# Kernel tuning notes

Hardware: AMD Instinct MI355X
Metric: run time of the kernel (lower is better)

## Reference

```python
import jax, jax.numpy as jnp
import numpy as np

K_TOP = 2  # top-k experts per token (MoE k)


def setup_inputs() -> dict:
    key = jax.random.key(0)
    ks = jax.random.split(key, 4)
    B, D, H, E = 4096, 1024, 2048, 8
    x = jax.random.normal(ks[0], (B, D), dtype=jnp.float32)
    w_gate = jax.random.normal(ks[1], (D, E), dtype=jnp.float32) * 0.02
    W1 = jax.random.normal(ks[2], (E, D, H), dtype=jnp.float32) * (1.0 / np.sqrt(D))
    b1 = jnp.zeros((E, H), dtype=jnp.float32)
    W2 = jax.random.normal(ks[3], (E, H, D), dtype=jnp.float32) * (1.0 / np.sqrt(H))
    b2 = jnp.zeros((E, D), dtype=jnp.float32)
    return {"x": x, "w_gate": w_gate, "W1": W1, "b1": b1, "W2": W2, "b2": b2}


def _top_k_gates(logits, k):
    # noisy_top_k_gating, eval path (noisy_gating=False / train=False):
    # softmax over the top-k logits, scattered back to [B, E]; other gates are 0.
    B, E = logits.shape
    top_logits, top_idx = jax.lax.top_k(logits, k)       # [B, k]
    top_gates = jax.nn.softmax(top_logits, axis=-1)      # [B, k]
    rows = jnp.arange(B)[:, None]
    gates = jnp.zeros((B, E), dtype=logits.dtype).at[rows, top_idx].set(top_gates)
    return gates


def reference(x, w_gate, W1, b1, W2, b2):
    # Gating
    logits = x @ w_gate                                  # [B, E]
    gates = _top_k_gates(logits, K_TOP)                  # [B, E], sparse (top-k nonzero)
    # Experts: MLP(fc1 -> relu -> fc2) per expert. Dense-all-experts form is
    # mathematically identical to dispatch/combine since zero gates contribute 0.
    h = jax.nn.relu(jnp.einsum('bd,edh->beh', x, W1) + b1[None])   # [B, E, H]
    y = jnp.einsum('beh,ehd->bed', h, W2) + b2[None]               # [B, E, D]
    out = jnp.einsum('be,bed->bd', gates, y)                       # gated scatter-combine
    return out
```

## Files before the change

### kernel.cpp

```cpp
#include <hip/hip_runtime.h>

#define B_TOK 4096
#define DDIM  1024
#define HDIM  2048
#define NEXP  8
#define MAXTOK 4096
#define BK 64
#define BM1 64
#define BN1 128
#define BM2 64
#define BN2 128

#define OFF_W1T  0ull
#define OFF_W2T  33554432ull
#define OFF_XB   67108864ull
#define OFF_H    75497472ull
#define OFF_Y    109051904ull
#define OFF_TOK  125829120ull
#define OFF_GATE 125960192ull
#define OFF_PAIR 126091264ull
#define OFF_CNT  126124032ull
#define OFF_OFFS 126124096ull
#define OFF_EIDX (OFF_Y)
#define OFF_GCO  (OFF_Y + 16384ull)

typedef __attribute__((ext_vector_type(4))) float f32x4;
typedef __attribute__((ext_vector_type(8))) short bf16x8;

static __device__ __forceinline__ unsigned short f2bf(float f) {
    unsigned u = __builtin_bit_cast(unsigned, f);
    unsigned r = (u + 0x7FFFu + ((u >> 16) & 1u)) >> 16;
    return (unsigned short)r;
}
static __device__ __forceinline__ float bf2f(unsigned short s) {
    unsigned u = ((unsigned)s) << 16;
    return __builtin_bit_cast(float, u);
}

#define AS1(p) ((const __attribute__((address_space(1))) void*)(p))
#define AS3(p) ((__attribute__((address_space(3))) void*)(p))

__global__ void __launch_bounds__(256) gating_logits_kernel(
    const float* __restrict__ x, const float* __restrict__ wg,
    int* __restrict__ eidx, float* __restrict__ gco, short* __restrict__ Xb) {
    int wave = threadIdx.x >> 6;
    int lane = threadIdx.x & 63;
    int b = blockIdx.x * 4 + wave;
    float acc[NEXP];
#pragma unroll
    for (int e = 0; e < NEXP; e++) acc[e] = 0.f;
    const float* xr = x + (size_t)b * DDIM;
    short* xbr = Xb + (size_t)b * DDIM;
#pragma unroll
    for (int i = 0; i < DDIM / 64; i++) {
        int d = i * 64 + lane;
        float xv = xr[d];
        xbr[d] = (short)f2bf(xv);
        const float4* wrow = (const float4*)(wg + (size_t)d * NEXP);
        float4 w0 = wrow[0], w1 = wrow[1];
        acc[0] += xv * w0.x; acc[1] += xv * w0.y; acc[2] += xv * w0.z; acc[3] += xv * w0.w;
        acc[4] += xv * w1.x; acc[5] += xv * w1.y; acc[6] += xv * w1.z; acc[7] += xv * w1.w;
    }
#pragma unroll
    for (int off = 32; off >= 1; off >>= 1)
#pragma unroll
        for (int e = 0; e < NEXP; e++) acc[e] += __shfl_xor(acc[e], off);
    if (lane == 0) {
        int i1 = 0; float m1 = acc[0];
        for (int e = 1; e < NEXP; e++) if (acc[e] > m1) { m1 = acc[e]; i1 = e; }
        int i2 = (i1 == 0) ? 1 : 0; float m2 = -1e30f;
        for (int e = 0; e < NEXP; e++) { if (e == i1) continue; if (acc[e] > m2) { m2 = acc[e]; i2 = e; } }
        float g1 = 1.f / (1.f + expf(m2 - m1));
        eidx[b] = i1 | (i2 << 16);
        gco[b] = g1;
    }
}

__global__ void __launch_bounds__(256) build_kernel(
    const int* __restrict__ eidx, const float* __restrict__ gco,
    int* __restrict__ counts, int* __restrict__ tok,
    float* __restrict__ gate, int* __restrict__ pair) {
    __shared__ int lhist[NEXP];
    __shared__ int gbase[NEXP];
    int t = threadIdx.x;
    if (t < NEXP) lhist[t] = 0;
    __syncthreads();
    int b = blockIdx.x * 256 + t;
    int ep = eidx[b];
    int e1 = ep & 0xffff, e2 = ep >> 16;
    float g1 = gco[b], g2 = 1.f - g1;
    int l1 = atomicAdd(&lhist[e1], 1);
    int l2 = atomicAdd(&lhist[e2], 1);
    __syncthreads();
    if (t < NEXP) gbase[t] = atomicAdd(&counts[t], lhist[t]);
    __syncthreads();
    int s1 = gbase[e1] + l1, s2 = gbase[e2] + l2;
    tok[e1 * MAXTOK + s1] = b; gate[e1 * MAXTOK + s1] = g1; pair[b * 2 + 0] = e1 * MAXTOK + s1;
    tok[e2 * MAXTOK + s2] = b; gate[e2 * MAXTOK + s2] = g2; pair[b * 2 + 1] = e2 * MAXTOK + s2;
}

__global__ void scan_kernel(const int* __restrict__ counts, int* __restrict__ offs) {
    if (threadIdx.x == 0) {
        int s = 0;
        for (int e = 0; e < NEXP; e++) { offs[e] = s; s += counts[e]; }
    }
}

__global__ void __launch_bounds__(256) tcvt_kernel(const float* __restrict__ src, short* __restrict__ dst,
                                                   int R, int C) {
    __shared__ float tile[64][65];
    int e = blockIdx.z;
    size_t base = (size_t)e * R * C;
    int r0 = blockIdx.y * 64, c0 = blockIdx.x * 64;
    int t = threadIdx.x;
    int rr = t >> 4, c4 = (t & 15) * 4;
    const float* s = src + base + (size_t)r0 * C + c0;
#pragma unroll
    for (int i = 0; i < 4; i++) {
        float4 v = *(const float4*)(s + (size_t)(rr + i * 16) * C + c4);
        tile[rr + i * 16][c4 + 0] = v.x; tile[rr + i * 16][c4 + 1] = v.y;
        tile[rr + i * 16][c4 + 2] = v.z; tile[rr + i * 16][c4 + 3] = v.w;
    }
    __syncthreads();
    short* d = dst + base + (size_t)c0 * R + r0;
    int hr0 = t >> 4, dc = (t & 15) * 4;
#pragma unroll
    for (int i = 0; i < 4; i++) {
        int hr = hr0 + i * 16;
        short4 o;
        o.x = (short)f2bf(tile[dc + 0][hr]); o.y = (short)f2bf(tile[dc + 1][hr]);
        o.z = (short)f2bf(tile[dc + 2][hr]); o.w = (short)f2bf(tile[dc + 3][hr]);
        *(short4*)(d + (size_t)hr * R + dc) = o;
    }
}

__global__ void __launch_bounds__(256, 4) fc1_kernel(
    const short* __restrict__ Xb, const short* __restrict__ W1T, const float* __restrict__ b1,
    short* __restrict__ h, const int* __restrict__ tok,
    const int* __restrict__ counts, const int* __restrict__ offs) {
    int bid = blockIdx.x;
    int e = bid & 7;
    int r2 = bid >> 3;
    int m0 = (r2 & 63) * BM1;
    int n0 = (r2 >> 6) * BN1;
    int cnt = counts[e];
    if (m0 >= cnt) return;
    int baseh = offs[e];

    __shared__ short As[BM1 * BK];
    __shared__ short Bs[BN1 * BK];

    int t = threadIdx.x;
    int wave = t >> 6, lane = t & 63;

    const short* asrc[2]; int dstoA[2];
    const short* bsrc[4]; int dstoB[4];
#pragma unroll
    for (int i = 0; i < 2; i++) {
        int G = i * 256 + t;
        int r = G >> 3, q = G & 7;
        int cks = ((q ^ (r & 7)) << 3);
        int trow = m0 + r;
        int tid2 = (trow < cnt) ? tok[e * MAXTOK + trow] : 0;
        asrc[i] = Xb + (size_t)tid2 * DDIM + cks;
        dstoA[i] = G * 8;
    }
#pragma unroll
    for (int i = 0; i < 4; i++) {
        int G = i * 256 + t;
        int r = G >> 3, q = G & 7;
        int cks = ((q ^ (r & 7)) << 3);
        bsrc[i] = W1T + ((size_t)e * HDIM + n0 + r) * DDIM + cks;
        dstoB[i] = G * 8;
    }

    int wr = (wave >> 1) * 32, wc = (wave & 1) * 64;
    f32x4 acc[2][4];
    f32x4 zero = {0.f, 0.f, 0.f, 0.f};
#pragma unroll
    for (int m = 0; m < 2; m++)
#pragma unroll
        for (int n = 0; n < 4; n++) acc[m][n] = zero;

    int l15 = lane & 15, l7 = lane & 7, lhi = lane >> 4;
    int aoff[2][2], boff[4][2];
#pragma unroll
    for (int ks = 0; ks < 2; ks++) {
        int q = (lhi + ks * 4) ^ l7;
#pragma unroll
        for (int m = 0; m < 2; m++) aoff[m][ks] = (wr + m * 16 + l15) * BK + (q << 3);
#pragma unroll
        for (int n = 0; n < 4; n++) boff[n][ks] = (wc + n * 16 + l15) * BK + (q << 3);
    }

    const int NT = DDIM / BK;
    for (int kt = 0; kt < NT; ++kt) {
        int k0 = kt * BK;
#pragma unroll
        for (int i = 0; i < 2; i++)
            __builtin_amdgcn_global_load_lds(AS1(asrc[i] + k0), AS3(&As[dstoA[i]]), 16, 0, 0);
#pragma unroll
        for (int i = 0; i < 4; i++)
            __builtin_amdgcn_global_load_lds(AS1(bsrc[i] + k0), AS3(&Bs[dstoB[i]]), 16, 0, 0);
        __syncthreads();
#pragma unroll
        for (int ks = 0; ks < 2; ks++) {
            bf16x8 af[2], bg[4];
#pragma unroll
            for (int m = 0; m < 2; m++) af[m] = *(const bf16x8*)(&As[aoff[m][ks]]);
#pragma unroll
            for (int n = 0; n < 4; n++) bg[n] = *(const bf16x8*)(&Bs[boff[n][ks]]);
            __builtin_amdgcn_s_setprio(1);
#pragma unroll
            for (int m = 0; m < 2; m++)
#pragma unroll
                for (int n = 0; n < 4; n++)
                    acc[m][n] = __builtin_amdgcn_mfma_f32_16x16x32_bf16(bg[n], af[m], acc[m][n], 0, 0, 0);
            __builtin_amdgcn_s_setprio(0);
        }
        __syncthreads();
    }

#pragma unroll
    for (int m = 0; m < 2; m++) {
        int row = m0 + wr + m * 16 + l15;
        if (row < cnt) {
            size_t rb = (size_t)(baseh + row) * HDIM;
#pragma unroll
            for (int n = 0; n < 4; n++) {
                int colb = n0 + wc + n * 16 + (lhi << 2);
                float4 bias = *(const float4*)(b1 + e * HDIM + colb);
                float v0 = acc[m][n][0] + bias.x; v0 = v0 > 0.f ? v0 : 0.f;
                float v1 = acc[m][n][1] + bias.y; v1 = v1 > 0.f ? v1 : 0.f;
                float v2 = acc[m][n][2] + bias.z; v2 = v2 > 0.f ? v2 : 0.f;
                float v3 = acc[m][n][3] + bias.w; v3 = v3 > 0.f ? v3 : 0.f;
                short4 o;
                o.x = (short)f2bf(v0); o.y = (short)f2bf(v1);
                o.z = (short)f2bf(v2); o.w = (short)f2bf(v3);
                *(short4*)(h + rb + colb) = o;
            }
        }
    }
}

__global__ void __launch_bounds__(256, 4) fc2_kernel(
    const short* __restrict__ h, const short* __restrict__ W2T, const float* __restrict__ b2,
    short* __restrict__ ybuf, const int* __restrict__ counts, const int* __restrict__ offs) {
    int bid = blockIdx.x;
    int e = bid & 7;
    int r2 = bid >> 3;
    int m0 = (r2 & 63) * BM2;
    int n0 = (r2 >> 6) * BN2;
    int cnt = counts[e];
    if (m0 >= cnt) return;
    int baseh = offs[e];

    __shared__ short As[BM2 * BK];
    __shared__ short Bs[BN2 * BK];

    int t = threadIdx.x;
    int wave = t >> 6, lane = t & 63;

    const short* asrc[2]; int dstoA[2];
    const short* bsrc[4]; int dstoB[4];
#pragma unroll
    for (int i = 0; i < 2; i++) {
        int G = i * 256 + t;
        int r = G >> 3, q = G & 7;
        int cks = ((q ^ (r & 7)) << 3);
        asrc[i] = h + (size_t)(baseh + m0 + r) * HDIM + cks;
        dstoA[i] = G * 8;
    }
#pragma unroll
    for (int i = 0; i < 4; i++) {
        int G = i * 256 + t;
        int r = G >> 3, q = G & 7;
        int cks = ((q ^ (r & 7)) << 3);
        bsrc[i] = W2T + ((size_t)e * DDIM + n0 + r) * HDIM + cks;
        dstoB[i] = G * 8;
    }

    int wr = (wave >> 1) * 32, wc = (wave & 1) * 64;
    f32x4 acc[2][4];
    f32x4 zero = {0.f, 0.f, 0.f, 0.f};
#pragma unroll
    for (int m = 0; m < 2; m++)
#pragma unroll
        for (int n = 0; n < 4; n++) acc[m][n] = zero;

    int l15 = lane & 15, l7 = lane & 7, lhi = lane >> 4;
    int aoff[2][2], boff[4][2];
#pragma unroll
    for (int ks = 0; ks < 2; ks++) {
        int q = (lhi + ks * 4) ^ l7;
#pragma unroll
        for (int m = 0; m < 2; m++) aoff[m][ks] = (wr + m * 16 + l15) * BK + (q << 3);
#pragma unroll
        for (int n = 0; n < 4; n++) boff[n][ks] = (wc + n * 16 + l15) * BK + (q << 3);
    }

    const int NT = HDIM / BK;
    for (int kt = 0; kt < NT; ++kt) {
        int k0 = kt * BK;
#pragma unroll
        for (int i = 0; i < 2; i++)
            __builtin_amdgcn_global_load_lds(AS1(asrc[i] + k0), AS3(&As[dstoA[i]]), 16, 0, 0);
#pragma unroll
        for (int i = 0; i < 4; i++)
            __builtin_amdgcn_global_load_lds(AS1(bsrc[i] + k0), AS3(&Bs[dstoB[i]]), 16, 0, 0);
        __syncthreads();
#pragma unroll
        for (int ks = 0; ks < 2; ks++) {
            bf16x8 af[2], bg[4];
#pragma unroll
            for (int m = 0; m < 2; m++) af[m] = *(const bf16x8*)(&As[aoff[m][ks]]);
#pragma unroll
            for (int n = 0; n < 4; n++) bg[n] = *(const bf16x8*)(&Bs[boff[n][ks]]);
            __builtin_amdgcn_s_setprio(1);
#pragma unroll
            for (int m = 0; m < 2; m++)
#pragma unroll
                for (int n = 0; n < 4; n++)
                    acc[m][n] = __builtin_amdgcn_mfma_f32_16x16x32_bf16(bg[n], af[m], acc[m][n], 0, 0, 0);
            __builtin_amdgcn_s_setprio(0);
        }
        __syncthreads();
    }

#pragma unroll
    for (int m = 0; m < 2; m++) {
        int row = m0 + wr + m * 16 + l15;
        if (row < cnt) {
            size_t rb = (size_t)(baseh + row) * DDIM;
#pragma unroll
            for (int n = 0; n < 4; n++) {
                int colb = n0 + wc + n * 16 + (lhi << 2);
                float4 bias = *(const float4*)(b2 + e * DDIM + colb);
                short4 o;
                o.x = (short)f2bf(acc[m][n][0] + bias.x);
                o.y = (short)f2bf(acc[m][n][1] + bias.y);
                o.z = (short)f2bf(acc[m][n][2] + bias.z);
                o.w = (short)f2bf(acc[m][n][3] + bias.w);
                *(short4*)(ybuf + rb + colb) = o;
            }
        }
    }
}

__global__ void __launch_bounds__(256) combine_kernel(
    const short* __restrict__ ybuf, const float* __restrict__ gate,
    const int* __restrict__ pair, const int* __restrict__ offs, float* __restrict__ out) {
    int b = blockIdx.x;
    int p0 = pair[b * 2], p1 = pair[b * 2 + 1];
    float g0 = gate[p0], g1 = gate[p1];
    int r0 = offs[p0 >> 12] + (p0 & 4095);
    int r1 = offs[p1 >> 12] + (p1 & 4095);
    const short4* y0 = (const short4*)(ybuf + (size_t)r0 * DDIM);
    const short4* y1 = (const short4*)(ybuf + (size_t)r1 * DDIM);
    float4* o = (float4*)(out + (size_t)b * DDIM);
    int t = threadIdx.x;
    short4 a = y0[t], c = y1[t];
    float4 v;
    v.x = g0 * bf2f((unsigned short)a.x) + g1 * bf2f((unsigned short)c.x);
    v.y = g0 * bf2f((unsigned short)a.y) + g1 * bf2f((unsigned short)c.y);
    v.z = g0 * bf2f((unsigned short)a.z) + g1 * bf2f((unsigned short)c.z);
    v.w = g0 * bf2f((unsigned short)a.w) + g1 * bf2f((unsigned short)c.w);
    o[t] = v;
}

extern "C" void kernel_launch(void* const* d_in, const int* in_sizes, int n_in,
                              void* d_out, int out_size, void* d_ws, size_t ws_size,
                              hipStream_t stream) {
    const float* x  = (const float*)d_in[0];
    const float* wg = (const float*)d_in[1];
    const float* W1 = (const float*)d_in[2];
    const float* b1 = (const float*)d_in[3];
    const float* W2 = (const float*)d_in[4];
    const float* b2 = (const float*)d_in[5];
    float* out = (float*)d_out;
    char* ws = (char*)d_ws;

    short* W1T = (short*)(ws + OFF_W1T);
    short* W2T = (short*)(ws + OFF_W2T);
    short* Xb  = (short*)(ws + OFF_XB);
    short* h   = (short*)(ws + OFF_H);
    short* ybuf = (short*)(ws + OFF_Y);
    int* tok   = (int*)(ws + OFF_TOK);
    float* gate = (float*)(ws + OFF_GATE);
    int* pair  = (int*)(ws + OFF_PAIR);
    int* counts = (int*)(ws + OFF_CNT);
    int* offs  = (int*)(ws + OFF_OFFS);
    int* eidx  = (int*)(ws + OFF_EIDX);
    float* gco = (float*)(ws + OFF_GCO);

    hipMemsetAsync(counts, 0, 64, stream);
    gating_logits_kernel<<<B_TOK / 4, 256, 0, stream>>>(x, wg, eidx, gco, Xb);
    build_kernel<<<B_TOK / 256, 256, 0, stream>>>(eidx, gco, counts, tok, gate, pair);
    scan_kernel<<<1, 64, 0, stream>>>(counts, offs);
    tcvt_kernel<<<dim3(HDIM / 64, DDIM / 64, NEXP), 256, 0, stream>>>(W1, W1T, DDIM, HDIM);
    tcvt_kernel<<<dim3(DDIM / 64, HDIM / 64, NEXP), 256, 0, stream>>>(W2, W2T, HDIM, DDIM);
    fc1_kernel<<<NEXP * (MAXTOK / BM1) * (HDIM / BN1), 256, 0, stream>>>(Xb, W1T, b1, h, tok, counts, offs);
    fc2_kernel<<<NEXP * (MAXTOK / BM2) * (DDIM / BN2), 256, 0, stream>>>(h, W2T, b2, ybuf, counts, offs);
    combine_kernel<<<B_TOK, 256, 0, stream>>>(ybuf, gate, pair, offs, out);
}
```

Before: 174.2 us.

## Double-buffer LDS tiles in fc1 and fc2 GEMMs to overlap loads with MFMA

Both expert GEMM kernels now keep two LDS buffers per operand and issue the global-to-LDS loads for the next K tile before computing the current one. A partial vmcnt wait lets the prefetch stay in flight while the current tile is consumed, hiding global load latency behind MFMA work. LDS use per block doubles and the launch-bounds occupancy hint drops from 4 to 3 blocks per CU, which may reduce latency hiding from concurrent blocks.

```diff
diff --git a/kernel.cpp b/kernel.cpp
--- a/kernel.cpp
+++ b/kernel.cpp
@@ -134,7 +134,7 @@
     }
 }
 
-__global__ void __launch_bounds__(256, 4) fc1_kernel(
+__global__ void __launch_bounds__(256, 3) fc1_kernel(
     const short* __restrict__ Xb, const short* __restrict__ W1T, const float* __restrict__ b1,
     short* __restrict__ h, const int* __restrict__ tok,
     const int* __restrict__ counts, const int* __restrict__ offs) {
@@ -147,8 +147,8 @@
     if (m0 >= cnt) return;
     int baseh = offs[e];
 
-    __shared__ short As[BM1 * BK];
-    __shared__ short Bs[BN1 * BK];
+    __shared__ short As[2][BM1 * BK];
+    __shared__ short Bs[2][BN1 * BK];
 
     int t = threadIdx.x;
     int wave = t >> 6, lane = t & 63;
@@ -193,33 +193,49 @@
         for (int n = 0; n < 4; n++) boff[n][ks] = (wc + n * 16 + l15) * BK + (q << 3);
     }
 
+#define STAGEF1(buf, k0) do { \
+    _Pragma("unroll") \
+    for (int i = 0; i < 2; i++) \
+        __builtin_amdgcn_global_load_lds(AS1(asrc[i] + (k0)), AS3(&As[buf][dstoA[i]]), 16, 0, 0); \
+    _Pragma("unroll") \
+    for (int i = 0; i < 4; i++) \
+        __builtin_amdgcn_global_load_lds(AS1(bsrc[i] + (k0)), AS3(&Bs[buf][dstoB[i]]), 16, 0, 0); \
+} while (0)
+
+#define COMPUTEF1(cur) do { \
+    _Pragma("unroll") \
+    for (int ks = 0; ks < 2; ks++) { \
+        bf16x8 af[2], bg[4]; \
+        _Pragma("unroll") \
+        for (int m = 0; m < 2; m++) af[m] = *(const bf16x8*)(&As[cur][aoff[m][ks]]); \
+        _Pragma("unroll") \
+        for (int n = 0; n < 4; n++) bg[n] = *(const bf16x8*)(&Bs[cur][boff[n][ks]]); \
+        __builtin_amdgcn_s_setprio(1); \
+        _Pragma("unroll") \
+        for (int m = 0; m < 2; m++) \
+            _Pragma("unroll") \
+            for (int n = 0; n < 4; n++) \
+                acc[m][n] = __builtin_amdgcn_mfma_f32_16x16x32_bf16(bg[n], af[m], acc[m][n], 0, 0, 0); \
+        __builtin_amdgcn_s_setprio(0); \
+    } \
+} while (0)
+
+    STAGEF1(0, 0);
+    int cur = 0;
     const int NT = DDIM / BK;
-    for (int kt = 0; kt < NT; ++kt) {
-        int k0 = kt * BK;
-#pragma unroll
-        for (int i = 0; i < 2; i++)
-            __builtin_amdgcn_global_load_lds(AS1(asrc[i] + k0), AS3(&As[dstoA[i]]), 16, 0, 0);
-#pragma unroll
-        for (int i = 0; i < 4; i++)
-            __builtin_amdgcn_global_load_lds(AS1(bsrc[i] + k0), AS3(&Bs[dstoB[i]]), 16, 0, 0);
-        __syncthreads();
-#pragma unroll
-        for (int ks = 0; ks < 2; ks++) {
-            bf16x8 af[2], bg[4];
-#pragma unroll
-            for (int m = 0; m < 2; m++) af[m] = *(const bf16x8*)(&As[aoff[m][ks]]);
-#pragma unroll
-            for (int n = 0; n < 4; n++) bg[n] = *(const bf16x8*)(&Bs[boff[n][ks]]);
-            __builtin_amdgcn_s_setprio(1);
-#pragma unroll
-            for (int m = 0; m < 2; m++)
-#pragma unroll
-                for (int n = 0; n < 4; n++)
-                    acc[m][n] = __builtin_amdgcn_mfma_f32_16x16x32_bf16(bg[n], af[m], acc[m][n], 0, 0, 0);
-            __builtin_amdgcn_s_setprio(0);
-        }
-        __syncthreads();
-    }
+    for (int kt = 0; kt < NT - 1; ++kt) {
+        STAGEF1(cur ^ 1, (kt + 1) * BK);
+        asm volatile("s_waitcnt vmcnt(6)" ::: "memory");
+        __builtin_amdgcn_s_barrier();
+        COMPUTEF1(cur);
+        __builtin_amdgcn_s_barrier();
+        cur ^= 1;
+    }
+    asm volatile("s_waitcnt vmcnt(0)" ::: "memory");
+    __builtin_amdgcn_s_barrier();
+    COMPUTEF1(cur);
+#undef STAGEF1
+#undef COMPUTEF1
 
 #pragma unroll
     for (int m = 0; m < 2; m++) {
@@ -243,7 +259,7 @@
     }
 }
 
-__global__ void __launch_bounds__(256, 4) fc2_kernel(
+__global__ void __launch_bounds__(256, 3) fc2_kernel(
     const short* __restrict__ h, const short* __restrict__ W2T, const float* __restrict__ b2,
     short* __restrict__ ybuf, const int* __restrict__ counts, const int* __restrict__ offs) {
     int bid = blockIdx.x;
@@ -255,8 +271,8 @@
     if (m0 >= cnt) return;
     int baseh = offs[e];
 
-    __shared__ short As[BM2 * BK];
-    __shared__ short Bs[BN2 * BK];
+    __shared__ short As[2][BM2 * BK];
+    __shared__ short Bs[2][BN2 * BK];
 
     int t = threadIdx.x;
     int wave = t >> 6, lane = t & 63;
@@ -299,33 +315,49 @@
         for (int n = 0; n < 4; n++) boff[n][ks] = (wc + n * 16 + l15) * BK + (q << 3);
     }
 
+#define STAGEF2(buf, k0) do { \
+    _Pragma("unroll") \
+    for (int i = 0; i < 2; i++) \
+        __builtin_amdgcn_global_load_lds(AS1(asrc[i] + (k0)), AS3(&As[buf][dstoA[i]]), 16, 0, 0); \
+    _Pragma("unroll") \
+    for (int i = 0; i < 4; i++) \
+        __builtin_amdgcn_global_load_lds(AS1(bsrc[i] + (k0)), AS3(&Bs[buf][dstoB[i]]), 16, 0, 0); \
+} while (0)
+
+#define COMPUTEF2(cur) do { \
+    _Pragma("unroll") \
+    for (int ks = 0; ks < 2; ks++) { \
+        bf16x8 af[2], bg[4]; \
+        _Pragma("unroll") \
+        for (int m = 0; m < 2; m++) af[m] = *(const bf16x8*)(&As[cur][aoff[m][ks]]); \
+        _Pragma("unroll") \
+        for (int n = 0; n < 4; n++) bg[n] = *(const bf16x8*)(&Bs[cur][boff[n][ks]]); \
+        __builtin_amdgcn_s_setprio(1); \
+        _Pragma("unroll") \
+        for (int m = 0; m < 2; m++) \
+            _Pragma("unroll") \
+            for (int n = 0; n < 4; n++) \
+                acc[m][n] = __builtin_amdgcn_mfma_f32_16x16x32_bf16(bg[n], af[m], acc[m][n], 0, 0, 0); \
+        __builtin_amdgcn_s_setprio(0); \
+    } \
+} while (0)
+
+    STAGEF2(0, 0);
+    int cur = 0;
     const int NT = HDIM / BK;
-    for (int kt = 0; kt < NT; ++kt) {
-        int k0 = kt * BK;
-#pragma unroll
-        for (int i = 0; i < 2; i++)
-            __builtin_amdgcn_global_load_lds(AS1(asrc[i] + k0), AS3(&As[dstoA[i]]), 16, 0, 0);
-#pragma unroll
-        for (int i = 0; i < 4; i++)
-            __builtin_amdgcn_global_load_lds(AS1(bsrc[i] + k0), AS3(&Bs[dstoB[i]]), 16, 0, 0);
-        __syncthreads();
-#pragma unroll
-        for (int ks = 0; ks < 2; ks++) {
-            bf16x8 af[2], bg[4];
-#pragma unroll
-            for (int m = 0; m < 2; m++) af[m] = *(const bf16x8*)(&As[aoff[m][ks]]);
-#pragma unroll
-            for (int n = 0; n < 4; n++) bg[n] = *(const bf16x8*)(&Bs[boff[n][ks]]);
-            __builtin_amdgcn_s_setprio(1);
-#pragma unroll
-            for (int m = 0; m < 2; m++)
-#pragma unroll
-                for (int n = 0; n < 4; n++)
-                    acc[m][n] = __builtin_amdgcn_mfma_f32_16x16x32_bf16(bg[n], af[m], acc[m][n], 0, 0, 0);
-            __builtin_amdgcn_s_setprio(0);
-        }
-        __syncthreads();
-    }
+    for (int kt = 0; kt < NT - 1; ++kt) {
+        STAGEF2(cur ^ 1, (kt + 1) * BK);
+        asm volatile("s_waitcnt vmcnt(6)" ::: "memory");
+        __builtin_amdgcn_s_barrier();
+        COMPUTEF2(cur);
+        __builtin_amdgcn_s_barrier();
+        cur ^= 1;
+    }
+    asm volatile("s_waitcnt vmcnt(0)" ::: "memory");
+    __builtin_amdgcn_s_barrier();
+    COMPUTEF2(cur);
+#undef STAGEF2
+#undef COMPUTEF2
 
 #pragma unroll
     for (int m = 0; m < 2; m++) {
```

Result: slower. 186.7 us (+7.2%).

## Load A operand directly from global into registers, dropping A shared-memory tile

Applied to the files above, without the earlier changes.

Both expert GEMM kernels stop staging the activation (A) tile through LDS. Each wave now loads its own A fragments straight from global memory into registers, using per-lane row pointers (token-gathered rows for fc1). This cuts LDS use and LDS traffic, and launch bounds are raised from 4 to 6 blocks per SM to exploit that. The cost is that A rows are re-read by the two waves sharing the same rows, with less coalesced 16-byte loads, and the higher occupancy target puts more pressure on registers.

```diff
diff --git a/kernel.cpp b/kernel.cpp
--- a/kernel.cpp
+++ b/kernel.cpp
@@ -134,7 +134,7 @@
     }
 }
 
-__global__ void __launch_bounds__(256, 4) fc1_kernel(
+__global__ void __launch_bounds__(256, 6) fc1_kernel(
     const short* __restrict__ Xb, const short* __restrict__ W1T, const float* __restrict__ b1,
     short* __restrict__ h, const int* __restrict__ tok,
     const int* __restrict__ counts, const int* __restrict__ offs) {
@@ -147,24 +147,13 @@
     if (m0 >= cnt) return;
     int baseh = offs[e];
 
-    __shared__ short As[BM1 * BK];
     __shared__ short Bs[BN1 * BK];
 
     int t = threadIdx.x;
     int wave = t >> 6, lane = t & 63;
-
-    const short* asrc[2]; int dstoA[2];
+    int l15 = lane & 15, l7 = lane & 7, lhi = lane >> 4;
+
     const short* bsrc[4]; int dstoB[4];
-#pragma unroll
-    for (int i = 0; i < 2; i++) {
-        int G = i * 256 + t;
-        int r = G >> 3, q = G & 7;
-        int cks = ((q ^ (r & 7)) << 3);
-        int trow = m0 + r;
-        int tid2 = (trow < cnt) ? tok[e * MAXTOK + trow] : 0;
-        asrc[i] = Xb + (size_t)tid2 * DDIM + cks;
-        dstoA[i] = G * 8;
-    }
 #pragma unroll
     for (int i = 0; i < 4; i++) {
         int G = i * 256 + t;
@@ -175,6 +164,15 @@
     }
 
     int wr = (wave >> 1) * 32, wc = (wave & 1) * 64;
+
+    const short* aptr[2];
+#pragma unroll
+    for (int m = 0; m < 2; m++) {
+        int row = m0 + wr + m * 16 + l15;
+        int tid2 = (row < cnt) ? tok[e * MAXTOK + row] : 0;
+        aptr[m] = Xb + (size_t)tid2 * DDIM + lhi * 8;
+    }
+
     f32x4 acc[2][4];
     f32x4 zero = {0.f, 0.f, 0.f, 0.f};
 #pragma unroll
@@ -182,13 +180,10 @@
 #pragma unroll
         for (int n = 0; n < 4; n++) acc[m][n] = zero;
 
-    int l15 = lane & 15, l7 = lane & 7, lhi = lane >> 4;
-    int aoff[2][2], boff[4][2];
+    int boff[4][2];
 #pragma unroll
     for (int ks = 0; ks < 2; ks++) {
         int q = (lhi + ks * 4) ^ l7;
-#pragma unroll
-        for (int m = 0; m < 2; m++) aoff[m][ks] = (wr + m * 16 + l15) * BK + (q << 3);
 #pragma unroll
         for (int n = 0; n < 4; n++) boff[n][ks] = (wc + n * 16 + l15) * BK + (q << 3);
     }
@@ -197,17 +192,18 @@
     for (int kt = 0; kt < NT; ++kt) {
         int k0 = kt * BK;
 #pragma unroll
-        for (int i = 0; i < 2; i++)
-            __builtin_amdgcn_global_load_lds(AS1(asrc[i] + k0), AS3(&As[dstoA[i]]), 16, 0, 0);
-#pragma unroll
         for (int i = 0; i < 4; i++)
             __builtin_amdgcn_global_load_lds(AS1(bsrc[i] + k0), AS3(&Bs[dstoB[i]]), 16, 0, 0);
+        bf16x8 af[2][2];
+#pragma unroll
+        for (int ks = 0; ks < 2; ks++)
+#pragma unroll
+            for (int m = 0; m < 2; m++)
+                af[m][ks] = *(const bf16x8*)(aptr[m] + k0 + ks * 32);
         __syncthreads();
 #pragma unroll
         for (int ks = 0; ks < 2; ks++) {
-            bf16x8 af[2], bg[4];
-#pragma unroll
-            for (int m = 0; m < 2; m++) af[m] = *(const bf16x8*)(&As[aoff[m][ks]]);
+            bf16x8 bg[4];
 #pragma unroll
             for (int n = 0; n < 4; n++) bg[n] = *(const bf16x8*)(&Bs[boff[n][ks]]);
             __builtin_amdgcn_s_setprio(1);
@@ -215,7 +211,7 @@
             for (int m = 0; m < 2; m++)
 #pragma unroll
                 for (int n = 0; n < 4; n++)
-                    acc[m][n] = __builtin_amdgcn_mfma_f32_16x16x32_bf16(bg[n], af[m], acc[m][n], 0, 0, 0);
+                    acc[m][n] = __builtin_amdgcn_mfma_f32_16x16x32_bf16(bg[n], af[m][ks], acc[m][n], 0, 0, 0);
             __builtin_amdgcn_s_setprio(0);
         }
         __syncthreads();
@@ -243,7 +239,7 @@
     }
 }
 
-__global__ void __launch_bounds__(256, 4) fc2_kernel(
+__global__ void __launch_bounds__(256, 6) fc2_kernel(
     const short* __restrict__ h, const short* __restrict__ W2T, const float* __restrict__ b2,
     short* __restrict__ ybuf, const int* __restrict__ counts, const int* __restrict__ offs) {
     int bid = blockIdx.x;
@@ -255,22 +251,13 @@
     if (m0 >= cnt) return;
     int baseh = offs[e];
 
-    __shared__ short As[BM2 * BK];
     __shared__ short Bs[BN2 * BK];
 
     int t = threadIdx.x;
     int wave = t >> 6, lane = t & 63;
-
-    const short* asrc[2]; int dstoA[2];
+    int l15 = lane & 15, l7 = lane & 7, lhi = lane >> 4;
+
     const short* bsrc[4]; int dstoB[4];
-#pragma unroll
-    for (int i = 0; i < 2; i++) {
-        int G = i * 256 + t;
-        int r = G >> 3, q = G & 7;
-        int cks = ((q ^ (r & 7)) << 3);
-        asrc[i] = h + (size_t)(baseh + m0 + r) * HDIM + cks;
-        dstoA[i] = G * 8;
-    }
 #pragma unroll
     for (int i = 0; i < 4; i++) {
         int G = i * 256 + t;
@@ -281,6 +268,14 @@
     }
 
     int wr = (wave >> 1) * 32, wc = (wave & 1) * 64;
+
+    const short* aptr[2];
+#pragma unroll
+    for (int m = 0; m < 2; m++) {
+        int row = m0 + wr + m * 16 + l15;
+        aptr[m] = h + (size_t)(baseh + row) * HDIM + lhi * 8;
+    }
+
     f32x4 acc[2][4];
     f32x4 zero = {0.f, 0.f, 0.f, 0.f};
 #pragma unroll
@@ -288,13 +283,10 @@
 #pragma unroll
         for (int n = 0; n < 4; n++) acc[m][n] = zero;
 
-    int l15 = lane & 15, l7 = lane & 7, lhi = lane >> 4;
-    int aoff[2][2], boff[4][2];
+    int boff[4][2];
 #pragma unroll
     for (int ks = 0; ks < 2; ks++) {
         int q = (lhi + ks * 4) ^ l7;
-#pragma unroll
-        for (int m = 0; m < 2; m++) aoff[m][ks] = (wr + m * 16 + l15) * BK + (q << 3);
 #pragma unroll
         for (int n = 0; n < 4; n++) boff[n][ks] = (wc + n * 16 + l15) * BK + (q << 3);
     }
@@ -303,17 +295,18 @@
     for (int kt = 0; kt < NT; ++kt) {
         int k0 = kt * BK;
 #pragma unroll
-        for (int i = 0; i < 2; i++)
-            __builtin_amdgcn_global_load_lds(AS1(asrc[i] + k0), AS3(&As[dstoA[i]]), 16, 0, 0);
-#pragma unroll
         for (int i = 0; i < 4; i++)
             __builtin_amdgcn_global_load_lds(AS1(bsrc[i] + k0), AS3(&Bs[dstoB[i]]), 16, 0, 0);
+        bf16x8 af[2][2];
+#pragma unroll
+        for (int ks = 0; ks < 2; ks++)
+#pragma unroll
+            for (int m = 0; m < 2; m++)
+                af[m][ks] = *(const bf16x8*)(aptr[m] + k0 + ks * 32);
         __syncthreads();
 #pragma unroll
         for (int ks = 0; ks < 2; ks++) {
-            bf16x8 af[2], bg[4];
-#pragma unroll
-            for (int m = 0; m < 2; m++) af[m] = *(const bf16x8*)(&As[aoff[m][ks]]);
+            bf16x8 bg[4];
 #pragma unroll
             for (int n = 0; n < 4; n++) bg[n] = *(const bf16x8*)(&Bs[boff[n][ks]]);
             __builtin_amdgcn_s_setprio(1);
@@ -321,7 +314,7 @@
             for (int m = 0; m < 2; m++)
 #pragma unroll
                 for (int n = 0; n < 4; n++)
-                    acc[m][n] = __builtin_amdgcn_mfma_f32_16x16x32_bf16(bg[n], af[m], acc[m][n], 0, 0, 0);
+                    acc[m][n] = __builtin_amdgcn_mfma_f32_16x16x32_bf16(bg[n], af[m][ks], acc[m][n], 0, 0, 0);
             __builtin_amdgcn_s_setprio(0);
         }
         __syncthreads();
```

Measured after the change: 331.3 us. +90.1%, slower.
